# Optimization experiments

Hardware: AMD Instinct MI355X
Metric: run time of the kernel (lower is better)

The kernel has to match this reference:

```python
import jax, jax.numpy as jnp
import numpy as np


def fps(xyz, nsamples):
    # xyz: [B, N, 3] -> [B, nsamples] furthest-point-sample indices (int32)
    def single(p):
        N = p.shape[0]
        def step(carry, _):
            dists, last = carry
            d = jnp.sum((p - p[last]) ** 2, axis=-1)
            dists = jnp.minimum(dists, d)
            return (dists, jnp.argmax(dists).astype(jnp.int32)), last
        init = (jnp.full((N,), 1e10, p.dtype), jnp.int32(0))
        _, idx = jax.lax.scan(step, init, None, length=nsamples)
        return idx
    return jax.vmap(single)(xyz)


def bn_relu(x, g, b, m, v):
    # inference BatchNorm2d folded into scale/shift, then ReLU; x: [B,C,S,N]
    s = g * jax.lax.rsqrt(v + 1e-5)
    return jax.nn.relu(x * s[None, :, None, None] + (b - m * s)[None, :, None, None])


def setup_inputs() -> dict:
    key = jax.random.key(0)
    ks = jax.random.split(key, 6)
    B, N, C, S = 8, 16384, 64, 5
    return dict(
        fg_xyz=jax.random.normal(ks[0], (B, N, 3), jnp.float32),
        fg_features=jax.random.normal(ks[1], (B, C, N), jnp.float32),
        bg_xyz=jax.random.normal(ks[2], (B, N, 3), jnp.float32),
        bg_features=jax.random.normal(ks[3], (B, C, N), jnp.float32),
        w1=jax.random.normal(ks[4], (C, 2 * C), jnp.float32) * (1.0 / np.sqrt(2 * C)),
        g1=jnp.ones((C,), jnp.float32), b1=jnp.zeros((C,), jnp.float32),
        m1=jnp.zeros((C,), jnp.float32), v1=jnp.ones((C,), jnp.float32),
        w2=jax.random.normal(ks[5], (C, C), jnp.float32) * (1.0 / np.sqrt(C)),
        g2=jnp.ones((C,), jnp.float32), b2=jnp.zeros((C,), jnp.float32),
        m2=jnp.zeros((C,), jnp.float32), v2=jnp.ones((C,), jnp.float32),
        nsamples=5,
    )


def reference(fg_xyz, fg_features, bg_xyz, bg_features,
              w1, g1, b1, m1, v1, w2, g2, b2, m2, v2, nsamples):
    B, C, N = fg_features.shape
    S = nsamples
    # D-FPS sample S background points, gather their features: [B, C, S]
    idx = fps(bg_xyz, S)
    sample_bg = jnp.take_along_axis(
        bg_features, jnp.broadcast_to(idx[:, None, :], (B, C, S)), axis=2)
    fg_exp = fg_features[:, :, None, :]                           # [B, C, 1, N]
    # candidates = [fg itself, S sampled bg feats tiled over the N fg points]
    fused_origin = jnp.concatenate(
        [fg_exp, jnp.broadcast_to(sample_bg[:, :, :, None], (B, C, S, N))], axis=2)  # [B,C,S+1,N]
    # weight-net input: fg feature concatenated with each candidate along channels
    fusion_in = jnp.concatenate(
        [jnp.broadcast_to(fg_exp, (B, C, S + 1, N)), fused_origin], axis=1)          # [B,2C,S+1,N]
    h = bn_relu(jnp.einsum('oc,bcsn->bosn', w1, fusion_in), g1, b1, m1, v1)
    w = bn_relu(jnp.einsum('oc,bcsn->bosn', w2, h), g2, b2, m2, v2)                  # [B,C,S+1,N]
    final_feats = jnp.sum(w * fused_origin, axis=2, keepdims=True)                   # [B,C,1,N]
    return fg_xyz, final_feats
```

## Files before the change

kernel.cpp:

```cpp
#include <hip/hip_runtime.h>

#define B_ 8
#define N_ 16384
#define C_ 64
#define S_ 5

typedef float v4f __attribute__((ext_vector_type(4)));
typedef __bf16 v8bf __attribute__((ext_vector_type(8)));
typedef unsigned int v4u __attribute__((ext_vector_type(4)));

static __device__ __forceinline__ unsigned short f2bf(float f) {
    unsigned int u = __float_as_uint(f);
    u += 0x7fffu + ((u >> 16) & 1u);
    return (unsigned short)(u >> 16);
}
static __device__ __forceinline__ float bf2f(unsigned short s) {
    return __uint_as_float(((unsigned int)s) << 16);
}

__global__ __launch_bounds__(512) void fps_kernel(const float* __restrict__ xyz,
                                                  int* __restrict__ idx_out) {
    const int b = blockIdx.x;
    const float* p = xyz + (size_t)b * N_ * 3;
    const int t = threadIdx.x;
    const int PPT = N_ / 512;

    float px[PPT], py[PPT], pz[PPT], dist[PPT];
#pragma unroll
    for (int k = 0; k < PPT; ++k) {
        int i = t + k * 512;
        px[k] = p[i * 3 + 0];
        py[k] = p[i * 3 + 1];
        pz[k] = p[i * 3 + 2];
        dist[k] = 1e10f;
    }

    __shared__ float s_best[8];
    __shared__ int s_bidx[8];
    __shared__ int s_last;
    int last = 0;
    if (t == 0) idx_out[b * S_ + 0] = 0;

    for (int step = 1; step < S_; ++step) {
        const float lx = p[last * 3 + 0];
        const float ly = p[last * 3 + 1];
        const float lz = p[last * 3 + 2];
        float best = -1.0f;
        int bidx = 0;
#pragma unroll
        for (int k = 0; k < PPT; ++k) {
            float dx = px[k] - lx, dy = py[k] - ly, dz = pz[k] - lz;
            float d = dx * dx + dy * dy + dz * dz;
            float nd = fminf(dist[k], d);
            dist[k] = nd;
            if (nd > best) { best = nd; bidx = t + k * 512; }
        }
#pragma unroll
        for (int off = 32; off > 0; off >>= 1) {
            float ob = __shfl_down(best, off, 64);
            int oi = __shfl_down(bidx, off, 64);
            if (ob > best || (ob == best && oi < bidx)) { best = ob; bidx = oi; }
        }
        if ((t & 63) == 0) { s_best[t >> 6] = best; s_bidx[t >> 6] = bidx; }
        __syncthreads();
        if (t == 0) {
            float bb = s_best[0];
            int bi = s_bidx[0];
#pragma unroll
            for (int w = 1; w < 8; ++w) {
                if (s_best[w] > bb || (s_best[w] == bb && s_bidx[w] < bi)) {
                    bb = s_best[w];
                    bi = s_bidx[w];
                }
            }
            s_last = bi;
            idx_out[b * S_ + step] = bi;
        }
        __syncthreads();
        last = s_last;
        __syncthreads();
    }
}

__global__ __launch_bounds__(256) void prep_w(
    const float* __restrict__ w1, const float* __restrict__ g1, const float* __restrict__ b1,
    const float* __restrict__ m1, const float* __restrict__ v1,
    const float* __restrict__ w2, const float* __restrict__ g2, const float* __restrict__ b2,
    const float* __restrict__ m2, const float* __restrict__ v2,
    float* __restrict__ w1bs, float* __restrict__ bb1, float* __restrict__ bb2,
    unsigned short* __restrict__ wa_bf, unsigned short* __restrict__ wc_bf,
    unsigned short* __restrict__ w2_bf) {
    const int t = threadIdx.x;
    for (int i = t; i < 64 * 64; i += 256) {
        const int o = i >> 6, c = i & 63;
        const float s1 = g1[o] / sqrtf(v1[o] + 1e-5f);
        const float s2 = g2[o] / sqrtf(v2[o] + 1e-5f);
        const float a = s1 * w1[o * 128 + c];
        const float bb = s1 * w1[o * 128 + 64 + c];
        w1bs[o * 64 + c] = bb;
        wa_bf[o * 64 + c] = f2bf(a);
        wc_bf[o * 64 + c] = f2bf(a + bb);
        w2_bf[o * 64 + c] = f2bf(s2 * w2[o * 64 + c]);
    }
    if (t < 64) {
        const float s1 = g1[t] / sqrtf(v1[t] + 1e-5f);
        const float s2 = g2[t] / sqrtf(v2[t] + 1e-5f);
        bb1[t] = b1[t] - m1[t] * s1;
        bb2[t] = b2[t] - m2[t] * s2;
    }
}

__global__ __launch_bounds__(64) void prep_sbg(
    const float* __restrict__ bg_feat, const int* __restrict__ idx,
    const float* __restrict__ w1bs, const float* __restrict__ bb1,
    float* __restrict__ sbg, float* __restrict__ ebb) {
    const int b = blockIdx.x, j = blockIdx.y;
    const int o = threadIdx.x;
    const int id = idx[b * S_ + j];
    __shared__ float sf[64];
    sf[o] = bg_feat[(size_t)b * C_ * N_ + (size_t)o * N_ + id];
    __syncthreads();
    float acc = 0.f;
#pragma unroll
    for (int c = 0; c < 64; ++c) acc += w1bs[o * 64 + c] * sf[c];
    sbg[(b * S_ + j) * 64 + o] = sf[o];
    ebb[(b * S_ + j) * 64 + o] = acc + bb1[o];
}

#define PITCH 72

__global__ __launch_bounds__(256) void fusion_main(
    const float* __restrict__ fg_feat,
    const unsigned short* __restrict__ wa_bf, const unsigned short* __restrict__ wc_bf,
    const unsigned short* __restrict__ w2_bf,
    const float* __restrict__ bb1, const float* __restrict__ bb2,
    const float* __restrict__ ebb, const float* __restrict__ sbg,
    float* __restrict__ out) {
    __shared__ unsigned short Ft[64 * PITCH];
    __shared__ unsigned short Ht[64 * PITCH];

    const int t = threadIdx.x;
    const int b = blockIdx.y;
    const int n0 = blockIdx.x * 64;
    const float* Fg = fg_feat + (size_t)b * C_ * N_ + n0;

    {
        const int n = t & 63;
        const int cg = (t >> 6) * 16;
        v4u w0, w1v;
#pragma unroll
        for (int i = 0; i < 8; ++i) {
            unsigned short lo = f2bf(Fg[(size_t)(cg + 2 * i) * N_ + n]);
            unsigned short hi = f2bf(Fg[(size_t)(cg + 2 * i + 1) * N_ + n]);
            unsigned int packed = (unsigned int)lo | ((unsigned int)hi << 16);
            if (i < 4) w0[i] = packed; else w1v[i - 4] = packed;
        }
        *(v4u*)&Ft[n * PITCH + cg] = w0;
        *(v4u*)&Ft[n * PITCH + cg + 8] = w1v;
    }

    const int lane = t & 63;
    const int wv = t >> 6;
    const int o0 = wv * 16;
    const int m = lane & 15;
    const int q = lane >> 4;
    const int arow = o0 + m;

    v8bf aWa[2], aWc[2], aW2[2];
#pragma unroll
    for (int ks = 0; ks < 2; ++ks) {
        aWa[ks] = *(const v8bf*)&wa_bf[arow * 64 + ks * 32 + q * 8];
        aWc[ks] = *(const v8bf*)&wc_bf[arow * 64 + ks * 32 + q * 8];
        aW2[ks] = *(const v8bf*)&w2_bf[arow * 64 + ks * 32 + q * 8];
    }

    const int ob4 = o0 + 4 * q;
    const v4f bb1r = *(const v4f*)&bb1[ob4];
    const v4f bb2r = *(const v4f*)&bb2[ob4];
    v4f ebbr[5], sbgr[5];
#pragma unroll
    for (int j = 0; j < 5; ++j) {
        ebbr[j] = *(const v4f*)&ebb[(b * 5 + j) * 64 + ob4];
        sbgr[j] = *(const v4f*)&sbg[(b * 5 + j) * 64 + ob4];
    }

    __syncthreads();

    v8bf bF[4][2];
#pragma unroll
    for (int nb = 0; nb < 4; ++nb)
#pragma unroll
        for (int ks = 0; ks < 2; ++ks)
            bF[nb][ks] = *(const v8bf*)&Ft[(nb * 16 + m) * PITCH + ks * 32 + q * 8];

    v4f U[4], U0[4];
#pragma unroll
    for (int nb = 0; nb < 4; ++nb) {
        v4f z = {0.f, 0.f, 0.f, 0.f};
        z = __builtin_amdgcn_mfma_f32_16x16x32_bf16(aWa[0], bF[nb][0], z, 0, 0, 0);
        U[nb] = __builtin_amdgcn_mfma_f32_16x16x32_bf16(aWa[1], bF[nb][1], z, 0, 0, 0);
        v4f z2 = {0.f, 0.f, 0.f, 0.f};
        z2 = __builtin_amdgcn_mfma_f32_16x16x32_bf16(aWc[0], bF[nb][0], z2, 0, 0, 0);
        U0[nb] = __builtin_amdgcn_mfma_f32_16x16x32_bf16(aWc[1], bF[nb][1], z2, 0, 0, 0);
    }

    v4f acc[4];
#pragma unroll
    for (int nb = 0; nb < 4; ++nb) acc[nb] = (v4f){0.f, 0.f, 0.f, 0.f};

#pragma unroll
    for (int s = 0; s < 6; ++s) {
#pragma unroll
        for (int nb = 0; nb < 4; ++nb) {
            unsigned int lo, hi;
            {
                float h0 = (s == 0) ? (U0[nb][0] + bb1r[0]) : (U[nb][0] + ebbr[s - 1][0]);
                float h1 = (s == 0) ? (U0[nb][1] + bb1r[1]) : (U[nb][1] + ebbr[s - 1][1]);
                float h2 = (s == 0) ? (U0[nb][2] + bb1r[2]) : (U[nb][2] + ebbr[s - 1][2]);
                float h3 = (s == 0) ? (U0[nb][3] + bb1r[3]) : (U[nb][3] + ebbr[s - 1][3]);
                lo = (unsigned int)f2bf(fmaxf(h0, 0.f)) | ((unsigned int)f2bf(fmaxf(h1, 0.f)) << 16);
                hi = (unsigned int)f2bf(fmaxf(h2, 0.f)) | ((unsigned int)f2bf(fmaxf(h3, 0.f)) << 16);
            }
            unsigned long long v = (unsigned long long)lo | ((unsigned long long)hi << 32);
            *(unsigned long long*)&Ht[(nb * 16 + m) * PITCH + ob4] = v;
        }
        __syncthreads();

        v4f p[4];
#pragma unroll
        for (int nb = 0; nb < 4; ++nb) {
            v8bf h0 = *(const v8bf*)&Ht[(nb * 16 + m) * PITCH + q * 8];
            v8bf h1 = *(const v8bf*)&Ht[(nb * 16 + m) * PITCH + 32 + q * 8];
            v4f z = {0.f, 0.f, 0.f, 0.f};
            z = __builtin_amdgcn_mfma_f32_16x16x32_bf16(aW2[0], h0, z, 0, 0, 0);
            p[nb] = __builtin_amdgcn_mfma_f32_16x16x32_bf16(aW2[1], h1, z, 0, 0, 0);
        }
        __syncthreads();

#pragma unroll
        for (int nb = 0; nb < 4; ++nb) {
            if (s == 0) {
                unsigned long long fv = *(const unsigned long long*)&Ft[(nb * 16 + m) * PITCH + ob4];
#pragma unroll
                for (int r = 0; r < 4; ++r) {
                    float w = fmaxf(p[nb][r] + bb2r[r], 0.f);
                    acc[nb][r] += w * bf2f((unsigned short)(fv >> (16 * r)));
                }
            } else {
#pragma unroll
                for (int r = 0; r < 4; ++r) {
                    float w = fmaxf(p[nb][r] + bb2r[r], 0.f);
                    acc[nb][r] += w * sbgr[s - 1][r];
                }
            }
        }
    }

#pragma unroll
    for (int nb = 0; nb < 4; ++nb)
#pragma unroll
        for (int r = 0; r < 4; ++r)
            out[(size_t)b * C_ * N_ + (size_t)(ob4 + r) * N_ + (n0 + nb * 16 + m)] = acc[nb][r];
}

extern "C" void kernel_launch(void* const* d_in, const int* in_sizes, int n_in,
                              void* d_out, int out_size, void* d_ws, size_t ws_size,
                              hipStream_t stream) {
    const float* fg_xyz = (const float*)d_in[0];
    const float* fg_feat = (const float*)d_in[1];
    const float* bg_xyz = (const float*)d_in[2];
    const float* bg_feat = (const float*)d_in[3];
    const float* w1 = (const float*)d_in[4];
    const float* g1 = (const float*)d_in[5];
    const float* b1 = (const float*)d_in[6];
    const float* m1 = (const float*)d_in[7];
    const float* v1 = (const float*)d_in[8];
    const float* w2 = (const float*)d_in[9];
    const float* g2 = (const float*)d_in[10];
    const float* b2 = (const float*)d_in[11];
    const float* m2 = (const float*)d_in[12];
    const float* v2 = (const float*)d_in[13];

    float* ws = (float*)d_ws;
    int* idx = (int*)(ws + 0);
    float* w1bs = ws + 64;
    float* ebb = w1bs + 4096;
    float* sbg = ebb + 2560;
    float* bb1 = sbg + 2560;
    float* bb2 = bb1 + 64;
    unsigned short* wa_bf = (unsigned short*)(bb2 + 64);
    unsigned short* wc_bf = wa_bf + 4096;
    unsigned short* w2_bf = wc_bf + 4096;

    float* out_feats = (float*)d_out + (size_t)B_ * N_ * 3;

    hipMemcpyAsync(d_out, d_in[0], (size_t)B_ * N_ * 3 * sizeof(float),
                   hipMemcpyDeviceToDevice, stream);

    fps_kernel<<<B_, 512, 0, stream>>>(bg_xyz, idx);
    prep_w<<<1, 256, 0, stream>>>(w1, g1, b1, m1, v1, w2, g2, b2, m2, v2,
                                  w1bs, bb1, bb2, wa_bf, wc_bf, w2_bf);
    prep_sbg<<<dim3(B_, S_), 64, 0, stream>>>(bg_feat, idx, w1bs, bb1, sbg, ebb);
    fusion_main<<<dim3(N_ / 64, B_), 256, 0, stream>>>(
        fg_feat, wa_bf, wc_bf, w2_bf, bb1, bb2, ebb, sbg, out_feats);
}
```

Before: 168.4 us.

## Fuse xyz copy into weight prep, FPS with bg gather, and remap fusion waves

The device-to-device memcpy of fg_xyz is folded into the weight-prep kernel as 96 extra copy blocks. The FPS kernel now also gathers the sampled bg features and computes ebb/sbg, removing the separate prep_sbg launch and the idx round trip through global memory. In fusion_main each wave now owns 16 points across all 64 output channels, using per-wave double-buffered H tiles. This drops the block-wide __syncthreads in the 6-step loop, at the cost of holding four times as many weight registers per lane.

```diff
diff --git a/kernel.cpp b/kernel.cpp
--- a/kernel.cpp
+++ b/kernel.cpp
@@ -18,79 +18,24 @@
     return __uint_as_float(((unsigned int)s) << 16);
 }
 
-__global__ __launch_bounds__(512) void fps_kernel(const float* __restrict__ xyz,
-                                                  int* __restrict__ idx_out) {
-    const int b = blockIdx.x;
-    const float* p = xyz + (size_t)b * N_ * 3;
-    const int t = threadIdx.x;
-    const int PPT = N_ / 512;
-
-    float px[PPT], py[PPT], pz[PPT], dist[PPT];
-#pragma unroll
-    for (int k = 0; k < PPT; ++k) {
-        int i = t + k * 512;
-        px[k] = p[i * 3 + 0];
-        py[k] = p[i * 3 + 1];
-        pz[k] = p[i * 3 + 2];
-        dist[k] = 1e10f;
-    }
-
-    __shared__ float s_best[8];
-    __shared__ int s_bidx[8];
-    __shared__ int s_last;
-    int last = 0;
-    if (t == 0) idx_out[b * S_ + 0] = 0;
-
-    for (int step = 1; step < S_; ++step) {
-        const float lx = p[last * 3 + 0];
-        const float ly = p[last * 3 + 1];
-        const float lz = p[last * 3 + 2];
-        float best = -1.0f;
-        int bidx = 0;
-#pragma unroll
-        for (int k = 0; k < PPT; ++k) {
-            float dx = px[k] - lx, dy = py[k] - ly, dz = pz[k] - lz;
-            float d = dx * dx + dy * dy + dz * dz;
-            float nd = fminf(dist[k], d);
-            dist[k] = nd;
-            if (nd > best) { best = nd; bidx = t + k * 512; }
-        }
-#pragma unroll
-        for (int off = 32; off > 0; off >>= 1) {
-            float ob = __shfl_down(best, off, 64);
-            int oi = __shfl_down(bidx, off, 64);
-            if (ob > best || (ob == best && oi < bidx)) { best = ob; bidx = oi; }
-        }
-        if ((t & 63) == 0) { s_best[t >> 6] = best; s_bidx[t >> 6] = bidx; }
-        __syncthreads();
-        if (t == 0) {
-            float bb = s_best[0];
-            int bi = s_bidx[0];
-#pragma unroll
-            for (int w = 1; w < 8; ++w) {
-                if (s_best[w] > bb || (s_best[w] == bb && s_bidx[w] < bi)) {
-                    bb = s_best[w];
-                    bi = s_bidx[w];
-                }
-            }
-            s_last = bi;
-            idx_out[b * S_ + step] = bi;
-        }
-        __syncthreads();
-        last = s_last;
-        __syncthreads();
-    }
-}
-
-__global__ __launch_bounds__(256) void prep_w(
+__global__ __launch_bounds__(256) void prep_w_copy(
     const float* __restrict__ w1, const float* __restrict__ g1, const float* __restrict__ b1,
     const float* __restrict__ m1, const float* __restrict__ v1,
     const float* __restrict__ w2, const float* __restrict__ g2, const float* __restrict__ b2,
     const float* __restrict__ m2, const float* __restrict__ v2,
     float* __restrict__ w1bs, float* __restrict__ bb1, float* __restrict__ bb2,
     unsigned short* __restrict__ wa_bf, unsigned short* __restrict__ wc_bf,
-    unsigned short* __restrict__ w2_bf) {
+    unsigned short* __restrict__ w2_bf,
+    const float* __restrict__ fg_xyz, float* __restrict__ out_xyz) {
     const int t = threadIdx.x;
+    const int blk = blockIdx.x;
+    if (blk > 0) {
+        const float4* src = (const float4*)(fg_xyz + (size_t)(blk - 1) * 4096);
+        float4* dst = (float4*)(out_xyz + (size_t)(blk - 1) * 4096);
+#pragma unroll
+        for (int i = 0; i < 4; ++i) dst[t + i * 256] = src[t + i * 256];
+        return;
+    }
     for (int i = t; i < 64 * 64; i += 256) {
         const int o = i >> 6, c = i & 63;
         const float s1 = g1[o] / sqrtf(v1[o] + 1e-5f);
@@ -110,21 +55,91 @@
     }
 }
 
-__global__ __launch_bounds__(64) void prep_sbg(
-    const float* __restrict__ bg_feat, const int* __restrict__ idx,
+__global__ __launch_bounds__(512) void fps_sbg(
+    const float* __restrict__ xyz, const float* __restrict__ bg_feat,
     const float* __restrict__ w1bs, const float* __restrict__ bb1,
     float* __restrict__ sbg, float* __restrict__ ebb) {
-    const int b = blockIdx.x, j = blockIdx.y;
-    const int o = threadIdx.x;
-    const int id = idx[b * S_ + j];
-    __shared__ float sf[64];
-    sf[o] = bg_feat[(size_t)b * C_ * N_ + (size_t)o * N_ + id];
+    const int b = blockIdx.x;
+    const float* p = xyz + (size_t)b * N_ * 3;
+    const int t = threadIdx.x;
+    const int PPT = N_ / 512;
+
+    float px[PPT], py[PPT], pz[PPT], dist[PPT];
+#pragma unroll
+    for (int k = 0; k < PPT; ++k) {
+        int i = t + k * 512;
+        px[k] = p[i * 3 + 0];
+        py[k] = p[i * 3 + 1];
+        pz[k] = p[i * 3 + 2];
+        dist[k] = 1e10f;
+    }
+
+    __shared__ float s_best[8];
+    __shared__ int s_bidx[8];
+    __shared__ int s_last;
+    __shared__ int s_idx[S_];
+    __shared__ float sf[S_][64];
+    int last = 0;
+    if (t == 0) s_idx[0] = 0;
+
+    for (int step = 1; step < S_; ++step) {
+        const float lx = p[last * 3 + 0];
+        const float ly = p[last * 3 + 1];
+        const float lz = p[last * 3 + 2];
+        float best = -1.0f;
+        int bidx = 0;
+#pragma unroll
+        for (int k = 0; k < PPT; ++k) {
+            float dx = px[k] - lx, dy = py[k] - ly, dz = pz[k] - lz;
+            float d = dx * dx + dy * dy + dz * dz;
+            float nd = fminf(dist[k], d);
+            dist[k] = nd;
+            if (nd > best) { best = nd; bidx = t + k * 512; }
+        }
+#pragma unroll
+        for (int off = 32; off > 0; off >>= 1) {
+            float ob = __shfl_down(best, off, 64);
+            int oi = __shfl_down(bidx, off, 64);
+            if (ob > best || (ob == best && oi < bidx)) { best = ob; bidx = oi; }
+        }
+        if ((t & 63) == 0) { s_best[t >> 6] = best; s_bidx[t >> 6] = bidx; }
+        __syncthreads();
+        if (t == 0) {
+            float bb = s_best[0];
+            int bi = s_bidx[0];
+#pragma unroll
+            for (int w = 1; w < 8; ++w) {
+                if (s_best[w] > bb || (s_best[w] == bb && s_bidx[w] < bi)) {
+                    bb = s_best[w];
+                    bi = s_bidx[w];
+                }
+            }
+            s_last = bi;
+            s_idx[step] = bi;
+        }
+        __syncthreads();
+        last = s_last;
+        __syncthreads();
+    }
+
+    if (t < S_ * 64) {
+        const int j = t >> 6, c = t & 63;
+        sf[j][c] = bg_feat[(size_t)b * C_ * N_ + (size_t)c * N_ + s_idx[j]];
+    }
     __syncthreads();
-    float acc = 0.f;
-#pragma unroll
-    for (int c = 0; c < 64; ++c) acc += w1bs[o * 64 + c] * sf[c];
-    sbg[(b * S_ + j) * 64 + o] = sf[o];
-    ebb[(b * S_ + j) * 64 + o] = acc + bb1[o];
+    if (t < S_ * 64) {
+        const int j = t >> 6, o = t & 63;
+        const float4* wr = (const float4*)&w1bs[o * 64];
+        float acc = 0.f;
+#pragma unroll
+        for (int c4 = 0; c4 < 16; ++c4) {
+            float4 wv = wr[c4];
+            acc += wv.x * sf[j][c4 * 4 + 0] + wv.y * sf[j][c4 * 4 + 1] +
+                   wv.z * sf[j][c4 * 4 + 2] + wv.w * sf[j][c4 * 4 + 3];
+        }
+        sbg[(b * S_ + j) * 64 + o] = sf[j][o];
+        ebb[(b * S_ + j) * 64 + o] = acc + bb1[o];
+    }
 }
 
 #define PITCH 72
@@ -133,11 +148,15 @@
     const float* __restrict__ fg_feat,
     const unsigned short* __restrict__ wa_bf, const unsigned short* __restrict__ wc_bf,
     const unsigned short* __restrict__ w2_bf,
-    const float* __restrict__ bb1, const float* __restrict__ bb2,
-    const float* __restrict__ ebb, const float* __restrict__ sbg,
+    const float* __restrict__ bb1g, const float* __restrict__ bb2g,
+    const float* __restrict__ ebbg, const float* __restrict__ sbgg,
     float* __restrict__ out) {
-    __shared__ unsigned short Ft[64 * PITCH];
-    __shared__ unsigned short Ht[64 * PITCH];
+    __shared__ __align__(16) unsigned short Ft[64 * PITCH];
+    __shared__ __align__(16) unsigned short Ht[2][4][16 * PITCH];
+    __shared__ __align__(16) float cEbb[S_ * 64];
+    __shared__ __align__(16) float cSbg[S_ * 64];
+    __shared__ __align__(16) float cBb1[64];
+    __shared__ __align__(16) float cBb2[64];
 
     const int t = threadIdx.x;
     const int b = blockIdx.y;
@@ -158,109 +177,104 @@
         *(v4u*)&Ft[n * PITCH + cg] = w0;
         *(v4u*)&Ft[n * PITCH + cg + 8] = w1v;
     }
+    for (int i = t; i < S_ * 64; i += 256) {
+        cEbb[i] = ebbg[b * (S_ * 64) + i];
+        cSbg[i] = sbgg[b * (S_ * 64) + i];
+    }
+    if (t < 64) { cBb1[t] = bb1g[t]; cBb2[t] = bb2g[t]; }
 
     const int lane = t & 63;
-    const int wv = t >> 6;
-    const int o0 = wv * 16;
+    const int w = t >> 6;
     const int m = lane & 15;
     const int q = lane >> 4;
-    const int arow = o0 + m;
-
-    v8bf aWa[2], aWc[2], aW2[2];
-#pragma unroll
-    for (int ks = 0; ks < 2; ++ks) {
-        aWa[ks] = *(const v8bf*)&wa_bf[arow * 64 + ks * 32 + q * 8];
-        aWc[ks] = *(const v8bf*)&wc_bf[arow * 64 + ks * 32 + q * 8];
-        aW2[ks] = *(const v8bf*)&w2_bf[arow * 64 + ks * 32 + q * 8];
-    }
-
-    const int ob4 = o0 + 4 * q;
-    const v4f bb1r = *(const v4f*)&bb1[ob4];
-    const v4f bb2r = *(const v4f*)&bb2[ob4];
-    v4f ebbr[5], sbgr[5];
-#pragma unroll
-    for (int j = 0; j < 5; ++j) {
-        ebbr[j] = *(const v4f*)&ebb[(b * 5 + j) * 64 + ob4];
-        sbgr[j] = *(const v4f*)&sbg[(b * 5 + j) * 64 + ob4];
-    }
+    const int nrow = w * 16 + m;
+
+    v8bf aWa[4][2], aWc[4][2], aW2[4][2];
+#pragma unroll
+    for (int ob = 0; ob < 4; ++ob)
+#pragma unroll
+        for (int ks = 0; ks < 2; ++ks) {
+            const int widx = (ob * 16 + m) * 64 + ks * 32 + q * 8;
+            aWa[ob][ks] = *(const v8bf*)&wa_bf[widx];
+            aWc[ob][ks] = *(const v8bf*)&wc_bf[widx];
+            aW2[ob][ks] = *(const v8bf*)&w2_bf[widx];
+        }
 
     __syncthreads();
 
-    v8bf bF[4][2];
-#pragma unroll
-    for (int nb = 0; nb < 4; ++nb)
-#pragma unroll
-        for (int ks = 0; ks < 2; ++ks)
-            bF[nb][ks] = *(const v8bf*)&Ft[(nb * 16 + m) * PITCH + ks * 32 + q * 8];
+    v8bf bF[2];
+#pragma unroll
+    for (int ks = 0; ks < 2; ++ks)
+        bF[ks] = *(const v8bf*)&Ft[nrow * PITCH + ks * 32 + q * 8];
 
     v4f U[4], U0[4];
 #pragma unroll
-    for (int nb = 0; nb < 4; ++nb) {
+    for (int ob = 0; ob < 4; ++ob) {
         v4f z = {0.f, 0.f, 0.f, 0.f};
-        z = __builtin_amdgcn_mfma_f32_16x16x32_bf16(aWa[0], bF[nb][0], z, 0, 0, 0);
-        U[nb] = __builtin_amdgcn_mfma_f32_16x16x32_bf16(aWa[1], bF[nb][1], z, 0, 0, 0);
+        z = __builtin_amdgcn_mfma_f32_16x16x32_bf16(aWa[ob][0], bF[0], z, 0, 0, 0);
+        U[ob] = __builtin_amdgcn_mfma_f32_16x16x32_bf16(aWa[ob][1], bF[1], z, 0, 0, 0);
         v4f z2 = {0.f, 0.f, 0.f, 0.f};
-        z2 = __builtin_amdgcn_mfma_f32_16x16x32_bf16(aWc[0], bF[nb][0], z2, 0, 0, 0);
-        U0[nb] = __builtin_amdgcn_mfma_f32_16x16x32_bf16(aWc[1], bF[nb][1], z2, 0, 0, 0);
+        z2 = __builtin_amdgcn_mfma_f32_16x16x32_bf16(aWc[ob][0], bF[0], z2, 0, 0, 0);
+        U0[ob] = __builtin_amdgcn_mfma_f32_16x16x32_bf16(aWc[ob][1], bF[1], z2, 0, 0, 0);
     }
 
     v4f acc[4];
 #pragma unroll
-    for (int nb = 0; nb < 4; ++nb) acc[nb] = (v4f){0.f, 0.f, 0.f, 0.f};
+    for (int ob = 0; ob < 4; ++ob) acc[ob] = (v4f){0.f, 0.f, 0.f, 0.f};
 
 #pragma unroll
     for (int s = 0; s < 6; ++s) {
-#pragma unroll
-        for (int nb = 0; nb < 4; ++nb) {
-            unsigned int lo, hi;
-            {
-                float h0 = (s == 0) ? (U0[nb][0] + bb1r[0]) : (U[nb][0] + ebbr[s - 1][0]);
-                float h1 = (s == 0) ? (U0[nb][1] + bb1r[1]) : (U[nb][1] + ebbr[s - 1][1]);
-                float h2 = (s == 0) ? (U0[nb][2] + bb1r[2]) : (U[nb][2] + ebbr[s - 1][2]);
-                float h3 = (s == 0) ? (U0[nb][3] + bb1r[3]) : (U[nb][3] + ebbr[s - 1][3]);
-                lo = (unsigned int)f2bf(fmaxf(h0, 0.f)) | ((unsigned int)f2bf(fmaxf(h1, 0.f)) << 16);
-                hi = (unsigned int)f2bf(fmaxf(h2, 0.f)) | ((unsigned int)f2bf(fmaxf(h3, 0.f)) << 16);
-            }
+        unsigned short* h = &Ht[s & 1][w][0];
+
+#pragma unroll
+        for (int ob = 0; ob < 4; ++ob) {
+            const int o4 = ob * 16 + 4 * q;
+            v4f cv, u;
+            if (s == 0) { cv = *(const v4f*)&cBb1[o4]; u = U0[ob]; }
+            else        { cv = *(const v4f*)&cEbb[(s - 1) * 64 + o4]; u = U[ob]; }
+            unsigned int lo = (unsigned int)f2bf(fmaxf(u[0] + cv[0], 0.f)) |
+                              ((unsigned int)f2bf(fmaxf(u[1] + cv[1], 0.f)) << 16);
+            unsigned int hi = (unsigned int)f2bf(fmaxf(u[2] + cv[2], 0.f)) |
+                              ((unsigned int)f2bf(fmaxf(u[3] + cv[3], 0.f)) << 16);
             unsigned long long v = (unsigned long long)lo | ((unsigned long long)hi << 32);
-            *(unsigned long long*)&Ht[(nb * 16 + m) * PITCH + ob4] = v;
-        }
-        __syncthreads();
-
-        v4f p[4];
-#pragma unroll
-        for (int nb = 0; nb < 4; ++nb) {
-            v8bf h0 = *(const v8bf*)&Ht[(nb * 16 + m) * PITCH + q * 8];
-            v8bf h1 = *(const v8bf*)&Ht[(nb * 16 + m) * PITCH + 32 + q * 8];
+            *(unsigned long long*)&h[m * PITCH + o4] = v;
+        }
+
+        v8bf hb0 = *(const v8bf*)&h[m * PITCH + q * 8];
+        v8bf hb1 = *(const v8bf*)&h[m * PITCH + 32 + q * 8];
+
+#pragma unroll
+        for (int ob = 0; ob < 4; ++ob) {
             v4f z = {0.f, 0.f, 0.f, 0.f};
-            z = __builtin_amdgcn_mfma_f32_16x16x32_bf16(aW2[0], h0, z, 0, 0, 0);
-            p[nb] = __builtin_amdgcn_mfma_f32_16x16x32_bf16(aW2[1], h1, z, 0, 0, 0);
-        }
-        __syncthreads();
-
-#pragma unroll
-        for (int nb = 0; nb < 4; ++nb) {
+            z = __builtin_amdgcn_mfma_f32_16x16x32_bf16(aW2[ob][0], hb0, z, 0, 0, 0);
+            v4f p = __builtin_amdgcn_mfma_f32_16x16x32_bf16(aW2[ob][1], hb1, z, 0, 0, 0);
+
+            const int o4 = ob * 16 + 4 * q;
+            const v4f b2v = *(const v4f*)&cBb2[o4];
             if (s == 0) {
-                unsigned long long fv = *(const unsigned long long*)&Ft[(nb * 16 + m) * PITCH + ob4];
+                unsigned long long fv = *(const unsigned long long*)&Ft[nrow * PITCH + o4];
 #pragma unroll
                 for (int r = 0; r < 4; ++r) {
-                    float w = fmaxf(p[nb][r] + bb2r[r], 0.f);
-                    acc[nb][r] += w * bf2f((unsigned short)(fv >> (16 * r)));
+                    float wgt = fmaxf(p[r] + b2v[r], 0.f);
+                    acc[ob][r] += wgt * bf2f((unsigned short)(fv >> (16 * r)));
                 }
             } else {
+                const v4f sb = *(const v4f*)&cSbg[(s - 1) * 64 + o4];
 #pragma unroll
                 for (int r = 0; r < 4; ++r) {
-                    float w = fmaxf(p[nb][r] + bb2r[r], 0.f);
-                    acc[nb][r] += w * sbgr[s - 1][r];
+                    float wgt = fmaxf(p[r] + b2v[r], 0.f);
+                    acc[ob][r] += wgt * sb[r];
                 }
             }
         }
     }
 
 #pragma unroll
-    for (int nb = 0; nb < 4; ++nb)
+    for (int ob = 0; ob < 4; ++ob)
 #pragma unroll
         for (int r = 0; r < 4; ++r)
-            out[(size_t)b * C_ * N_ + (size_t)(ob4 + r) * N_ + (n0 + nb * 16 + m)] = acc[nb][r];
+            out[(size_t)b * C_ * N_ + (size_t)(ob * 16 + 4 * q + r) * N_ + (n0 + w * 16 + m)] =
+                acc[ob][r];
 }
 
 extern "C" void kernel_launch(void* const* d_in, const int* in_sizes, int n_in,
@@ -282,8 +296,7 @@
     const float* v2 = (const float*)d_in[13];
 
     float* ws = (float*)d_ws;
-    int* idx = (int*)(ws + 0);
-    float* w1bs = ws + 64;
+    float* w1bs = ws;
     float* ebb = w1bs + 4096;
     float* sbg = ebb + 2560;
     float* bb1 = sbg + 2560;
@@ -294,13 +307,10 @@
 
     float* out_feats = (float*)d_out + (size_t)B_ * N_ * 3;
 
-    hipMemcpyAsync(d_out, d_in[0], (size_t)B_ * N_ * 3 * sizeof(float),
-                   hipMemcpyDeviceToDevice, stream);
-
-    fps_kernel<<<B_, 512, 0, stream>>>(bg_xyz, idx);
-    prep_w<<<1, 256, 0, stream>>>(w1, g1, b1, m1, v1, w2, g2, b2, m2, v2,
-                                  w1bs, bb1, bb2, wa_bf, wc_bf, w2_bf);
-    prep_sbg<<<dim3(B_, S_), 64, 0, stream>>>(bg_feat, idx, w1bs, bb1, sbg, ebb);
+    prep_w_copy<<<97, 256, 0, stream>>>(w1, g1, b1, m1, v1, w2, g2, b2, m2, v2,
+                                        w1bs, bb1, bb2, wa_bf, wc_bf, w2_bf,
+                                        fg_xyz, (float*)d_out);
+    fps_sbg<<<B_, 512, 0, stream>>>(bg_xyz, bg_feat, w1bs, bb1, sbg, ebb);
     fusion_main<<<dim3(N_ / 64, B_), 256, 0, stream>>>(
         fg_feat, wa_bf, wc_bf, w2_bf, bb1, bb2, ebb, sbg, out_feats);
 }
```

Result: slower. 174.7 us (+3.7%).
